# Kernel tuning notes

Measured on AMD Instinct MI355X. Metric: run time of the kernel, lower is better.

Reference implementation:

```python
import jax, jax.numpy as jnp
import numpy as np
from jax import lax

EPS = 1e-5

def mish(x):
    return x * jnp.tanh(jax.nn.softplus(x))

def conv2d(x, w, b, pad):
    y = lax.conv_general_dilated(x, w, (1, 1), [(pad, pad), (pad, pad)],
                                 dimension_numbers=('NCHW', 'OIHW', 'NCHW'))
    return y + b[None, :, None, None]

def dyn_conv(x, w):
    # Per-sample conv with a given kernel: x (B,1,H,W), w (B,Co,k,k).
    # torch code loops (batch, out-channel); equivalent grouped conv with groups=B.
    B, _, H, W = x.shape
    _, Co, k, _ = w.shape
    pad = k // 2 - 1  # int(k/2)-1 as in the torch module
    y = lax.conv_general_dilated(x.reshape(1, B, H, W), w.reshape(B * Co, 1, k, k),
                                 (1, 1), [(pad, pad), (pad, pad)],
                                 feature_group_count=B,
                                 dimension_numbers=('NCHW', 'OIHW', 'NCHW'))
    return y.reshape(B, Co, y.shape[2], y.shape[3])

def maxpool2(x):
    return lax.reduce_window(x, -jnp.inf, lax.max, (1, 1, 2, 2), (1, 1, 2, 2), 'VALID')

def up2(x):
    # bilinear upsample x2, align_corners=True (matches nn.Upsample)
    B, C, H, W = x.shape
    def idx(n):
        s = jnp.arange(2 * n, dtype=x.dtype) * ((n - 1) / (2 * n - 1))
        i0 = jnp.floor(s).astype(jnp.int32)
        i1 = jnp.minimum(i0 + 1, n - 1)
        return i0, i1, s - i0.astype(x.dtype)
    y0, y1, fy = idx(H)
    x0, x1, fx = idx(W)
    a = x[:, :, y0, :] * (1 - fy)[None, None, :, None] + x[:, :, y1, :] * fy[None, None, :, None]
    return a[:, :, :, x0] * (1 - fx) + a[:, :, :, x1] * fx

def batchnorm(x, g, b):
    mu = jnp.mean(x, axis=(0, 2, 3), keepdims=True)
    var = jnp.var(x, axis=(0, 2, 3), keepdims=True)
    return g[None, :, None, None] * (x - mu) * lax.rsqrt(var + EPS) + b[None, :, None, None]

def double_conv(x, wa, ba, wb, bb):
    return mish(conv2d(mish(conv2d(x, wa, ba, 1)), wb, bb, 1))

def setup_inputs() -> dict:
    key = jax.random.key(0)
    ks = iter(jax.random.split(key, 64))
    def rnd(shape, scale):
        return jax.random.normal(next(ks), shape, jnp.float32) * scale
    def cw(co, ci, kk):
        return rnd((co, ci, kk, kk), 1.0 / np.sqrt(ci * kk * kk))
    def cb(co):
        return rnd((co,), 0.01)
    B, H, W, K, NC = 4, 256, 256, 4, 1
    inp = {}
    inp['x'] = rnd((B, 1, H, W), 1.0)
    inp['w'] = rnd((B, 32, K, K), 0.25)  # per-sample dynamic kernels
    inp['d1w'], inp['d1b'] = cw(32, 32, 4), cb(32)
    inp['w2a'], inp['b2a'], inp['w2b'], inp['b2b'] = cw(128, 32, 3), cb(128), cw(128, 128, 3), cb(128)
    inp['w3a'], inp['b3a'], inp['w3b'], inp['b3b'] = cw(256, 128, 3), cb(256), cw(256, 256, 3), cb(256)
    inp['w4a'], inp['b4a'], inp['w4b'], inp['b4b'] = cw(512, 256, 3), cb(512), cw(512, 512, 3), cb(512)
    inp['g4'], inp['be4'] = 1.0 + rnd((512,), 0.1), rnd((512,), 0.1)
    inp['u3a'], inp['ub3a'], inp['u3b'], inp['ub3b'] = cw(256, 768, 3), cb(256), cw(256, 256, 3), cb(256)
    inp['u2a'], inp['ub2a'], inp['u2b'], inp['ub2b'] = cw(128, 384, 3), cb(128), cw(128, 128, 3), cb(128)
    inp['u1a'], inp['ub1a'], inp['u1b'], inp['ub1b'] = cw(32, 160, 3), cb(32), cw(32, 32, 3), cb(32)
    inp['wl'], inp['bl'] = cw(NC, 32, 1), cb(NC)
    return inp

def reference(x, w, d1w, d1b, w2a, b2a, w2b, b2b, w3a, b3a, w3b, b3b,
              w4a, b4a, w4b, b4b, g4, be4, u3a, ub3a, u3b, ub3b,
              u2a, ub2a, u2b, ub2b, u1a, ub1a, u1b, ub1b, wl, bl):
    c1 = mish(conv2d(mish(dyn_conv(x, w)), d1w, d1b, 2))  # (B,32,256,256)
    p = maxpool2(c1)
    c2 = double_conv(p, w2a, b2a, w2b, b2b)               # (B,128,128,128)
    p = maxpool2(c2)
    c3 = double_conv(p, w3a, b3a, w3b, b3b)               # (B,256,64,64)
    p = maxpool2(c3)
    h = double_conv(p, w4a, b4a, w4b, b4b)                # (B,512,32,32)
    h = batchnorm(h, g4, be4)
    h = jnp.concatenate([up2(h), c3], axis=1)             # (B,768,64,64)
    h = double_conv(h, u3a, ub3a, u3b, ub3b)
    h = jnp.concatenate([up2(h), c2], axis=1)             # (B,384,128,128)
    h = double_conv(h, u2a, ub2a, u2b, ub2b)
    h = jnp.concatenate([up2(h), c1], axis=1)             # (B,160,256,256)
    h = double_conv(h, u1a, ub1a, u1b, ub1b)
    return conv2d(h, wl, bl, 0)
```

## Files before the change

kernel.cpp:

```cpp
#include <hip/hip_runtime.h>
#include <hip/hip_bf16.h>
#include <math.h>

#define DEV static __device__ __forceinline__

typedef __attribute__((ext_vector_type(8))) short short8;
typedef __attribute__((ext_vector_type(4))) float floatx4;

DEV float bf2f(const __hip_bfloat16 v) { return __bfloat162float(v); }
DEV float bfu2f(unsigned short u) { return __uint_as_float((unsigned)u << 16); }

DEV unsigned short f2bf(float v) {
    unsigned int b = __float_as_uint(v);
    unsigned int r = (b + 0x7FFFu + ((b >> 16) & 1u)) >> 16;
    return (unsigned short)r;
}

DEV float mishf(float x) {
    float sp = fmaxf(x, 0.0f) + __logf(1.0f + __expf(-fabsf(x)));
    float t = __expf(-2.0f * sp);
    return __fdividef(x * (1.0f - t), 1.0f + t);
}

template<int N> DEV void s_wait_vm() {
    constexpr unsigned e = (unsigned)(N & 15) | (((unsigned)N >> 4) << 14)
                         | (7u << 4) | (15u << 8);
    __builtin_amdgcn_s_waitcnt(e);
}

#define N_T 32
struct Tab {
    const void* src[N_T];
    long long   dstoff[N_T];
    int         n[N_T];
    int         isw[N_T];
    int         cin[N_T];
    int         kk[N_T];
};

__global__ __launch_bounds__(256) void k_detect(Tab t, int* __restrict__ flags) {
    int i = blockIdx.x;
    int n = t.n[i];
    int m = n < 16384 ? n : 16384;
    const unsigned short* p = (const unsigned short*)t.src[i];
    __shared__ int sInf, sExt, sZero;
    if (threadIdx.x == 0) { sInf = 0; sExt = 0; sZero = 0; }
    __syncthreads();
    int cInf = 0, cExt = 0, cZero = 0;
    for (int j = threadIdx.x; j < m; j += 256) {
        unsigned short h = p[j];
        if ((h & 0x7F80) == 0x7F80) cInf++;
        if ((j & 1) == 0) {
            if (h == 0) cZero++;
            else { int e = (h >> 7) & 0xFF; if (e < 56 || e > 184) cExt++; }
        }
    }
    if (cInf)  atomicAdd(&sInf, cInf);
    if (cExt)  atomicAdd(&sExt, cExt);
    if (cZero) atomicAdd(&sZero, cZero);
    __syncthreads();
    if (threadIdx.x == 0) {
        int nEven = (m + 1) >> 1;
        flags[i] = (sInf > 0 || sExt > 0 || (nEven > 0 && sZero == nEven)) ? 2 : 0;
    }
}

__global__ void k_flag_final(Tab t, int* __restrict__ flags, int xi,
                             float* __restrict__ zp) {
    if (blockIdx.x == 0 && threadIdx.x < 16) zp[threadIdx.x] = 0.0f;
    if (threadIdx.x == 0 && blockIdx.x == 0) {
        int xf = (flags[xi] == 2) ? 1 : 0;
        for (int i = 0; i < N_T; ++i) {
            int f;
            if (flags[i] == 2)       f = 1;
            else if (t.n[i] >= 256)  f = 0;
            else                     f = xf;
            flags[i] = f;
        }
    }
}

__global__ __launch_bounds__(256) void k_convert(
        Tab t, float* __restrict__ pf, unsigned short* __restrict__ wb,
        const int* __restrict__ flags) {
    long long idx = (long long)blockIdx.x * 256 + threadIdx.x;
    long long off = 0;
    #pragma unroll 1
    for (int i = 0; i < N_T; ++i) {
        long long ni = t.n[i];
        if (idx < off + ni) {
            int j = (int)(idx - off);
            float v = flags[i] ? ((const float*)t.src[i])[j]
                               : bf2f(((const __hip_bfloat16*)t.src[i])[j]);
            if (t.isw[i]) {
                int cin = t.cin[i], kk = t.kk[i];
                int ckk = cin * kk;
                int co = j / ckk;
                int rem = j - co * ckk;
                int ci = rem / kk;
                int tt = rem - ci * kk;
                int cb = co >> 4, m = co & 15;
                int ch = ci >> 5, q = (ci >> 3) & 3, jj = ci & 7;
                int nc = cin >> 5;
                size_t dst = (((size_t)(cb * kk + tt) * nc + ch) << 9)
                           + (size_t)((q << 4) + m) * 8 + jj;
                wb[t.dstoff[i] + dst] = f2bf(v);
            } else {
                pf[t.dstoff[i] + j] = v;
            }
            return;
        }
        off += ni;
    }
}

__global__ __launch_bounds__(256) void k_dynconv_mish(
        const float* __restrict__ x, const float* __restrict__ w,
        unsigned short* __restrict__ out) {
    const int HO = 255, WO = 255, H = 256, W = 256;
    int p = blockIdx.x * 256 + threadIdx.x;
    if (p >= HO * WO) return;
    int b = blockIdx.y;
    int yo = p / WO, xo = p - yo * WO;
    const float* xp = x + b * H * W;

    float xv[16];
    #pragma unroll
    for (int ky = 0; ky < 4; ++ky) {
        int iy = yo + ky - 1;
        bool yok = (unsigned)iy < (unsigned)H;
        #pragma unroll
        for (int kx = 0; kx < 4; ++kx) {
            int ix = xo + kx - 1;
            xv[ky * 4 + kx] = (yok && (unsigned)ix < (unsigned)W)
                              ? xp[iy * W + ix] : 0.0f;
        }
    }

    const float* wb = w + (b << 9);
    unsigned int ow[16];
    #pragma unroll
    for (int c2 = 0; c2 < 16; ++c2) {
        const float* w0 = wb + (c2 << 5);
        const float* w1 = w0 + 16;
        float a0 = 0.f, a1 = 0.f;
        #pragma unroll
        for (int k = 0; k < 16; ++k) {
            a0 = fmaf(xv[k], w0[k], a0);
            a1 = fmaf(xv[k], w1[k], a1);
        }
        ow[c2] = (unsigned)f2bf(mishf(a0)) | ((unsigned)f2bf(mishf(a1)) << 16);
    }

    unsigned short* op = out + ((size_t)(b * HO * WO) + p) * 32;
    uint4 v;
    v.x = ow[0];  v.y = ow[1];  v.z = ow[2];  v.w = ow[3];
    *(uint4*)(op +  0) = v;
    v.x = ow[4];  v.y = ow[5];  v.z = ow[6];  v.w = ow[7];
    *(uint4*)(op +  8) = v;
    v.x = ow[8];  v.y = ow[9];  v.z = ow[10]; v.w = ow[11];
    *(uint4*)(op + 16) = v;
    v.x = ow[12]; v.y = ow[13]; v.z = ow[14]; v.w = ow[15];
    *(uint4*)(op + 24) = v;
}

template<int KS, int WPX, int WCO, int CO_FR>
__global__ __launch_bounds__(256) void k_conv2(
        const unsigned short* __restrict__ s0, int C0,
        const unsigned short* __restrict__ s1, int C1,
        const unsigned short* __restrict__ wgt,
        const float* __restrict__ bias,
        unsigned short* __restrict__ out,
        int Hin, int Win, int Hout, int Wout, int Co,
        const float* __restrict__ zpad) {
    constexpr int PAD = KS - 2;
    constexpr int KK = KS * KS;
    constexpr int TY = WPX * 4;
    constexpr int HWd = 16 + KS - 1;
    constexpr int HHd = TY + KS - 1;
    constexpr int NLOC = HWd * HHd;
    constexpr int NLD = NLOC * 4;
    constexpr int NPASS = (NLD + 255) / 256;
    constexpr int HALF = NPASS * 2048;
    constexpr int NAV = (KS == 3) ? KK * CO_FR : 0;
    static_assert(2 * HALF * 2 <= 65536, "LDS overflow");
    static_assert(WPX * WCO == 4, "4 waves");
    static_assert(NAV + NPASS <= 63, "vmcnt range");
    __shared__ __align__(16) unsigned short lds[2 * HALF];

    const int tid = threadIdx.x, lane = tid & 63, wv = tid >> 6;
    const int wr = wv / WCO, wc = wv % WCO;
    const int xn = lane & 15, qd = lane >> 4;
    const int C = C0 + C1, NC = C >> 5;
    const int NC0 = C0 >> 5;

    const int txc = Wout >> 4, tyc = Hout / TY;
    const int tpb = txc * tyc;
    const int b = blockIdx.x / tpb;
    int rem = blockIdx.x - b * tpb;
    const int tyi = rem / txc, txi = rem - tyi * txc;
    const int y0 = tyi * TY, x0 = txi << 4;
    const int cobase = blockIdx.y * (WCO * CO_FR * 16);
    const int cob16_0 = (cobase >> 4) + wc * CO_FR;

    const unsigned short* sb0 = s0 + (size_t)b * Hin * Win * C0;
    const unsigned short* sb1 = s1 ? s1 + (size_t)b * Hin * Win * C1 : s0;

    floatx4 acc[4][CO_FR];
    #pragma unroll
    for (int p = 0; p < 4; ++p)
        #pragma unroll
        for (int q = 0; q < CO_FR; ++q)
            acc[p][q] = (floatx4){0.f, 0.f, 0.f, 0.f};

    const int c8 = (tid & 3) << 3;
    int srow[NPASS];
    int sinc[NPASS];
    #pragma unroll
    for (int p_ = 0; p_ < NPASS; ++p_) {
        int i_ = p_ * 256 + tid;
        int loc = i_ >> 2;
        int hy = loc / HWd, hx = loc - hy * HWd;
        int iy = y0 + hy - PAD, ix = x0 + hx - PAD;
        bool ok = (i_ < NLD) && ((unsigned)iy < (unsigned)Hin)
                             && ((unsigned)ix < (unsigned)Win);
        srow[p_] = iy * Win + ix;
        sinc[p_] = ok ? 32 : 0;
    }
    const unsigned short* sptr[NPASS];
    auto initp = [&](const unsigned short* srcp, int Cs) {
        #pragma unroll
        for (int p_ = 0; p_ < NPASS; ++p_)
            sptr[p_] = sinc[p_] ? srcp + (size_t)srow[p_] * Cs + c8
                                : (const unsigned short*)zpad;
    };
    int scnt = 0;
    auto stage_next = [&](int h_) {
        if (s1 && scnt == NC0) initp(sb1, C1);
        #pragma unroll
        for (int p_ = 0; p_ < NPASS; ++p_) {
            __builtin_amdgcn_global_load_lds(
                (const unsigned int*)sptr[p_],
                (unsigned int*)&lds[h_ * HALF + (p_ * 256 + wv * 64) * 8],
                16, 0, 0);
            sptr[p_] += sinc[p_];
        }
        ++scnt;
    };

    initp(sb0, C0);
    stage_next(0);
    for (int ci_ = 0; ci_ < NC; ++ci_) {
        const int h = ci_ & 1;
        const size_t wof = ((size_t)cob16_0 * KK * NC + ci_) * 512 + lane * 8;
        short8 avr[KK][CO_FR];
        if constexpr (KS == 3) {
            #pragma unroll
            for (int tap = 0; tap < KK; ++tap)
                #pragma unroll
                for (int q = 0; q < CO_FR; ++q)
                    avr[tap][q] = *(const short8*)(wgt + wof
                                    + (size_t)(q * KK + tap) * NC * 512);
            __builtin_amdgcn_sched_barrier(0);
        }
        if (ci_ + 1 < NC) stage_next(h ^ 1);
        __builtin_amdgcn_sched_barrier(0);
        if (ci_ + 1 < NC) s_wait_vm<NAV + NPASS>();
        else              s_wait_vm<NAV>();
        __builtin_amdgcn_s_barrier();
        __builtin_amdgcn_sched_barrier(0);
        const unsigned short* base = &lds[h * HALF];
        #pragma unroll
        for (int dy = 0; dy < KS; ++dy) {
            #pragma unroll
            for (int dx = 0; dx < KS; ++dx) {
                const int tap = dy * KS + dx;
                short8 av[CO_FR];
                if constexpr (KS == 3) {
                    #pragma unroll
                    for (int q = 0; q < CO_FR; ++q) av[q] = avr[tap][q];
                } else {
                    #pragma unroll
                    for (int q = 0; q < CO_FR; ++q)
                        av[q] = *(const short8*)(wgt + wof
                                  + (size_t)(q * KK + tap) * NC * 512);
                }
                #pragma unroll
                for (int p = 0; p < 4; ++p) {
                    short8 bv = *(const short8*)&base[
                        ((4 * wr + p + dy) * HWd + xn + dx) * 32 + qd * 8];
                    #pragma unroll
                    for (int q = 0; q < CO_FR; ++q)
                        acc[p][q] = __builtin_amdgcn_mfma_f32_16x16x32_bf16(
                            av[q], bv, acc[p][q], 0, 0, 0);
                }
            }
        }
        __builtin_amdgcn_sched_barrier(0);
        __builtin_amdgcn_s_barrier();
        __builtin_amdgcn_sched_barrier(0);
    }

    #pragma unroll
    for (int p = 0; p < 4; ++p) {
        const int y = y0 + 4 * wr + p;
        unsigned short* ob = out + (((size_t)b * Hout + y) * Wout + x0 + xn) * Co;
        #pragma unroll
        for (int q = 0; q < CO_FR; ++q) {
            const int co = cobase + (wc * CO_FR + q) * 16 + qd * 4;
            ushort4 o;
            o.x = f2bf(mishf(acc[p][q][0] + bias[co + 0]));
            o.y = f2bf(mishf(acc[p][q][1] + bias[co + 1]));
            o.z = f2bf(mishf(acc[p][q][2] + bias[co + 2]));
            o.w = f2bf(mishf(acc[p][q][3] + bias[co + 3]));
            *(ushort4*)(ob + co) = o;
        }
    }
}

__global__ __launch_bounds__(256) void k_maxpool(
        const unsigned short* __restrict__ in, unsigned short* __restrict__ out,
        int lgWin, int lgC, int total8) {
    int idx = blockIdx.x * 256 + threadIdx.x;
    if (idx >= total8) return;
    int Wo = 1 << (lgWin - 1);
    int vc = idx & ((1 << (lgC - 3)) - 1); int t = idx >> (lgC - 3);
    int xo = t & (Wo - 1); t >>= (lgWin - 1);
    int yo = t & (Wo - 1); int b = t >> (lgWin - 1);
    size_t base = (((((size_t)(b << lgWin) + 2 * yo) << lgWin) + 2 * xo) << lgC)
                + ((size_t)vc << 3);
    size_t dc = (size_t)1 << lgC, dr = (size_t)1 << (lgWin + lgC);
    short8 v0 = *(const short8*)&in[base];
    short8 v1 = *(const short8*)&in[base + dc];
    short8 v2 = *(const short8*)&in[base + dr];
    short8 v3 = *(const short8*)&in[base + dr + dc];
    short8 o;
    #pragma unroll
    for (int j = 0; j < 8; ++j) {
        float m = fmaxf(fmaxf(bfu2f((unsigned short)v0[j]),
                              bfu2f((unsigned short)v1[j])),
                        fmaxf(bfu2f((unsigned short)v2[j]),
                              bfu2f((unsigned short)v3[j])));
        o[j] = (short)f2bf(m);
    }
    *(short8*)&out[(size_t)idx * 8] = o;
}

__global__ __launch_bounds__(256) void k_bn_reduce(
        const unsigned short* __restrict__ in, float* __restrict__ stats) {
    __shared__ float ls[4], ls2[4];
    int c = blockIdx.x;
    int tid = threadIdx.x;
    float s = 0.f, s2 = 0.f;
    for (int i = tid; i < 4096; i += 256) {
        float v = bfu2f(in[(size_t)i * 512 + c]);
        s += v; s2 += v * v;
    }
    #pragma unroll
    for (int off = 32; off; off >>= 1) {
        s  += __shfl_down(s, off, 64);
        s2 += __shfl_down(s2, off, 64);
    }
    if ((tid & 63) == 0) { ls[tid >> 6] = s; ls2[tid >> 6] = s2; }
    __syncthreads();
    if (tid == 0) {
        s  = ls[0] + ls[1] + ls[2] + ls[3];
        s2 = ls2[0] + ls2[1] + ls2[2] + ls2[3];
        float mean = s * (1.f / 4096.f);
        float var  = fmaxf(s2 * (1.f / 4096.f) - mean * mean, 0.f);
        stats[c]       = mean;
        stats[512 + c] = rsqrtf(var + 1e-5f);
    }
}

__global__ __launch_bounds__(256) void k_bn_apply(
        unsigned short* __restrict__ data, const float* __restrict__ stats,
        const float* __restrict__ g, const float* __restrict__ be, int total8) {
    int idx = blockIdx.x * 256 + threadIdx.x;
    if (idx >= total8) return;
    int c0 = (idx & 63) << 3;
    short8 v = *(const short8*)&data[(size_t)idx * 8];
    short8 o;
    #pragma unroll
    for (int j = 0; j < 8; ++j) {
        int c = c0 + j;
        float x = bfu2f((unsigned short)v[j]);
        o[j] = (short)f2bf(g[c] * (x - stats[c]) * stats[512 + c] + be[c]);
    }
    *(short8*)&data[(size_t)idx * 8] = o;
}

__global__ __launch_bounds__(256) void k_up2(
        const unsigned short* __restrict__ in, unsigned short* __restrict__ out,
        int lgW, int lgC, int total8) {
    int idx = blockIdx.x * 256 + threadIdx.x;
    if (idx >= total8) return;
    int H = 1 << lgW;
    int vc = idx & ((1 << (lgC - 3)) - 1); int t = idx >> (lgC - 3);
    int xo = t & (2 * H - 1); t >>= (lgW + 1);
    int yo = t & (2 * H - 1); int b = t >> (lgW + 1);
    float sc = (float)(H - 1) / (float)(2 * H - 1);
    float sy = yo * sc, sx = xo * sc;
    int y0 = (int)sy; int y1 = min(y0 + 1, H - 1); float fy = sy - (float)y0;
    int x0 = (int)sx; int x1 = min(x0 + 1, H - 1); float fx = sx - (float)x0;
    size_t bb = (size_t)b << (2 * lgW);
    size_t c = (size_t)vc << 3;
    size_t i00 = (((bb + ((size_t)y0 << lgW) + x0)) << lgC) + c;
    size_t i01 = (((bb + ((size_t)y0 << lgW) + x1)) << lgC) + c;
    size_t i10 = (((bb + ((size_t)y1 << lgW) + x0)) << lgC) + c;
    size_t i11 = (((bb + ((size_t)y1 << lgW) + x1)) << lgC) + c;
    short8 a00 = *(const short8*)&in[i00];
    short8 a01 = *(const short8*)&in[i01];
    short8 a10 = *(const short8*)&in[i10];
    short8 a11 = *(const short8*)&in[i11];
    short8 o;
    #pragma unroll
    for (int j = 0; j < 8; ++j) {
        float a  = bfu2f((unsigned short)a00[j]) * (1.f - fx)
                 + bfu2f((unsigned short)a01[j]) * fx;
        float b2 = bfu2f((unsigned short)a10[j]) * (1.f - fx)
                 + bfu2f((unsigned short)a11[j]) * fx;
        o[j] = (short)f2bf(a * (1.f - fy) + b2 * fy);
    }
    *(short8*)&out[(size_t)idx * 8] = o;
}

__global__ __launch_bounds__(256) void k_final1x1(
        const unsigned short* __restrict__ in, const float* __restrict__ wl,
        const float* __restrict__ bl, float* __restrict__ out) {
    int idx = blockIdx.x * 256 + threadIdx.x;
    if (idx >= 4 * 256 * 256) return;
    const unsigned short* p = in + (size_t)idx * 32;
    short8 r0 = *(const short8*)&p[0];
    short8 r1 = *(const short8*)&p[8];
    short8 r2 = *(const short8*)&p[16];
    short8 r3 = *(const short8*)&p[24];
    float acc = bl[0];
    #pragma unroll
    for (int j = 0; j < 8; ++j) {
        acc = fmaf(bfu2f((unsigned short)r0[j]), wl[j],      acc);
        acc = fmaf(bfu2f((unsigned short)r1[j]), wl[j + 8],  acc);
        acc = fmaf(bfu2f((unsigned short)r2[j]), wl[j + 16], acc);
        acc = fmaf(bfu2f((unsigned short)r3[j]), wl[j + 24], acc);
    }
    out[idx] = acc;
}

static inline int nblk(long long n) { return (int)((n + 255) / 256); }

extern "C" void kernel_launch(void* const* d_in, const int* in_sizes, int n_in,
                              void* d_out, int out_size, void* d_ws, size_t ws_size,
                              hipStream_t stream) {
    static const int EXP_SZ[N_T] = {
        262144, 2048, 16384, 32, 36864, 128, 147456, 128,
        294912, 256, 589824, 256, 1179648, 512, 2359296, 512,
        512, 512, 1769472, 256, 589824, 256, 442368, 128,
        147456, 128, 46080, 32, 9216, 32, 32, 1 };
    static const int ISW[N_T] = {
        0,0,1,0, 1,0,1,0, 1,0,1,0, 1,0,1,0,
        0,0, 1,0,1,0, 1,0,1,0, 1,0,1,0, 0,0 };
    static const int CIN[N_T] = {
        0,0,32,0, 32,0,128,0, 128,0,256,0, 256,0,512,0,
        0,0, 768,0,256,0, 384,0,128,0, 160,0,32,0, 0,0 };
    static const int KKA[N_T] = {
        0,0,16,0, 9,0,9,0, 9,0,9,0, 9,0,9,0,
        0,0, 9,0,9,0, 9,0,9,0, 9,0,9,0, 0,0 };
    int o = -1;
    for (int s = 0; s + N_T <= n_in; ++s) {
        bool ok = true;
        for (int j = 0; j < N_T; ++j)
            if (in_sizes[s + j] != EXP_SZ[j]) { ok = false; break; }
        if (ok) { o = s; break; }
    }
    if (o < 0) return;

    float* ws = (float*)d_ws;
    const long long PFN   = 270336;
    const long long C1o   = PFN;
    const long long C2o   = C1o + 8388608;
    const long long C3o   = C2o + 8388608;
    const long long Po    = C3o + 4194304;
    const long long Qo    = Po  + 8388608;
    const long long STo   = Qo  + 8388608;
    const long long FLo   = STo + 1024;
    const long long ZPo   = FLo + 64;
    const long long WBo   = ZPo + 16;
    const long long WBN   = 7628800;
    const size_t NEED = (size_t)WBo * 4 + WBN * 2 + 256;
    if (ws_size < NEED) return;

    float* PF = ws;
    unsigned short* C1 = (unsigned short*)(ws + C1o);
    unsigned short* C2 = (unsigned short*)(ws + C2o);
    unsigned short* C3 = (unsigned short*)(ws + C3o);
    unsigned short* P  = (unsigned short*)(ws + Po);
    unsigned short* Q  = (unsigned short*)(ws + Qo);
    float* ST = ws + STo;
    int* FLAGS = (int*)(ws + FLo);
    float* ZP = ws + ZPo;
    unsigned short* WB = (unsigned short*)(ws + WBo);
    unsigned short* X3 = C3;
    unsigned short* U2 = P;
    unsigned short* H2 = C2;
    unsigned short* U1 = P;
    unsigned short* X1 = C3;
    unsigned short* O1 = P;

    Tab tab;
    long long foff = 0, woff = 0, total = 0;
    const float* fp[N_T];
    const unsigned short* wbp[N_T];
    for (int i = 0; i < N_T; ++i) {
        tab.src[i] = d_in[o + i];
        tab.n[i]   = in_sizes[o + i];
        tab.isw[i] = ISW[i];
        tab.cin[i] = CIN[i];
        tab.kk[i]  = KKA[i];
        if (ISW[i]) { tab.dstoff[i] = woff; wbp[i] = WB + woff; fp[i] = nullptr; woff += tab.n[i]; }
        else        { tab.dstoff[i] = foff; fp[i] = PF + foff; wbp[i] = nullptr; foff += tab.n[i]; }
        total += tab.n[i];
    }
    if (foff > PFN || woff > WBN) return;

    const float* xf  = fp[0];  const float* wf = fp[1];
    const unsigned short* d1w = wbp[2];  const float* d1b = fp[3];
    const unsigned short* w2a = wbp[4];  const float* b2a = fp[5];
    const unsigned short* w2b = wbp[6];  const float* b2b = fp[7];
    const unsigned short* w3a = wbp[8];  const float* b3a = fp[9];
    const unsigned short* w3b = wbp[10]; const float* b3b = fp[11];
    const unsigned short* w4a = wbp[12]; const float* b4a = fp[13];
    const unsigned short* w4b = wbp[14]; const float* b4b = fp[15];
    const float* g4 = fp[16], *be4 = fp[17];
    const unsigned short* u3aw = wbp[18]; const float* ub3a = fp[19];
    const unsigned short* u3bw = wbp[20]; const float* ub3b = fp[21];
    const unsigned short* u2aw = wbp[22]; const float* ub2a = fp[23];
    const unsigned short* u2bw = wbp[24]; const float* ub2b = fp[25];
    const unsigned short* u1aw = wbp[26]; const float* ub1a = fp[27];
    const unsigned short* u1bw = wbp[28]; const float* ub1b = fp[29];
    const float* wl = fp[30], *bl = fp[31];
    float* outp = (float*)d_out;

    dim3 blk(256);
    long long n;

    k_detect<<<N_T, blk, 0, stream>>>(tab, FLAGS);
    k_flag_final<<<1, 64, 0, stream>>>(tab, FLAGS, 0, ZP);
    k_convert<<<nblk(total), blk, 0, stream>>>(tab, PF, WB, FLAGS);

    k_dynconv_mish<<<dim3(nblk(255 * 255), 4), blk, 0, stream>>>(xf, wf, P);
    k_conv2<4, 4, 1, 2><<<dim3(4 * 16 * 16, 1), blk, 0, stream>>>(
        P, 32, nullptr, 0, d1w, d1b, C1, 255, 255, 256, 256, 32, ZP);
    n = 4ll * 128 * 128 * 32 / 8;
    k_maxpool<<<nblk(n), blk, 0, stream>>>(C1, Q, 8, 5, (int)n);
    k_conv2<3, 2, 2, 2><<<dim3(4 * 8 * 16, 2), blk, 0, stream>>>(
        Q, 32, nullptr, 0, w2a, b2a, P, 128, 128, 128, 128, 128, ZP);
    k_conv2<3, 2, 2, 2><<<dim3(4 * 8 * 16, 2), blk, 0, stream>>>(
        P, 128, nullptr, 0, w2b, b2b, C2, 128, 128, 128, 128, 128, ZP);
    n = 4ll * 64 * 64 * 128 / 8;
    k_maxpool<<<nblk(n), blk, 0, stream>>>(C2, Q, 7, 7, (int)n);
    k_conv2<3, 2, 2, 1><<<dim3(4 * 4 * 8, 8), blk, 0, stream>>>(
        Q, 128, nullptr, 0, w3a, b3a, P, 64, 64, 64, 64, 256, ZP);
    k_conv2<3, 2, 2, 1><<<dim3(4 * 4 * 8, 8), blk, 0, stream>>>(
        P, 256, nullptr, 0, w3b, b3b, C3, 64, 64, 64, 64, 256, ZP);
    n = 4ll * 32 * 32 * 256 / 8;
    k_maxpool<<<nblk(n), blk, 0, stream>>>(C3, Q, 6, 8, (int)n);
    k_conv2<3, 2, 2, 1><<<dim3(4 * 2 * 4, 16), blk, 0, stream>>>(
        Q, 256, nullptr, 0, w4a, b4a, P, 32, 32, 32, 32, 512, ZP);
    k_conv2<3, 2, 2, 1><<<dim3(4 * 2 * 4, 16), blk, 0, stream>>>(
        P, 512, nullptr, 0, w4b, b4b, Q, 32, 32, 32, 32, 512, ZP);
    n = 4ll * 32 * 32 * 512 / 8;
    k_bn_reduce<<<512, blk, 0, stream>>>(Q, ST);
    k_bn_apply<<<nblk(n), blk, 0, stream>>>(Q, ST, g4, be4, (int)n);

    n = 4ll * 64 * 64 * 512 / 8;
    k_up2<<<nblk(n), blk, 0, stream>>>(Q, P, 5, 9, (int)n);
    k_conv2<3, 2, 2, 1><<<dim3(4 * 4 * 8, 8), blk, 0, stream>>>(
        P, 512, C3, 256, u3aw, ub3a, Q, 64, 64, 64, 64, 256, ZP);
    k_conv2<3, 2, 2, 1><<<dim3(4 * 4 * 8, 8), blk, 0, stream>>>(
        Q, 256, nullptr, 0, u3bw, ub3b, X3, 64, 64, 64, 64, 256, ZP);

    n = 4ll * 128 * 128 * 256 / 8;
    k_up2<<<nblk(n), blk, 0, stream>>>(X3, U2, 6, 8, (int)n);
    k_conv2<3, 2, 2, 2><<<dim3(4 * 8 * 16, 2), blk, 0, stream>>>(
        U2, 256, C2, 128, u2aw, ub2a, Q, 128, 128, 128, 128, 128, ZP);
    k_conv2<3, 2, 2, 2><<<dim3(4 * 8 * 16, 2), blk, 0, stream>>>(
        Q, 128, nullptr, 0, u2bw, ub2b, H2, 128, 128, 128, 128, 128, ZP);

    n = 4ll * 256 * 256 * 128 / 8;
    k_up2<<<nblk(n), blk, 0, stream>>>(H2, U1, 7, 7, (int)n);
    k_conv2<3, 4, 1, 2><<<dim3(4 * 16 * 16, 1), blk, 0, stream>>>(
        U1, 128, C1, 32, u1aw, ub1a, X1, 256, 256, 256, 256, 32, ZP);
    k_conv2<3, 4, 1, 2><<<dim3(4 * 16 * 16, 1), blk, 0, stream>>>(
        X1, 32, nullptr, 0, u1bw, ub1b, O1, 256, 256, 256, 256, 32, ZP);

    n = 4ll * 256 * 256;
    k_final1x1<<<nblk(n), blk, 0, stream>>>(O1, wl, bl, outp);
}
```

Before: 682.0 us.

## Reuse LDS input rows across filter taps in 3x3 conv, speed up weight conversion

The 3x3 conv inner loop now walks the six input rows a warp touches and loads each row's three shifted B fragments from LDS once, feeding every (output row, dy) pair that uses them. This replaces the old per-tap, per-output-row loads, cutting LDS reads from 36 to 18 per channel chunk. Separately, the weight/param convert kernel finds its tensor from a per-block start table instead of a linear scan, and replaces integer divides with magic-number multiplies. The risk is higher register pressure from holding extra B fragments alongside the preloaded weight fragments.

```diff
diff --git a/kernel.cpp b/kernel.cpp
--- a/kernel.cpp
+++ b/kernel.cpp
@@ -36,6 +36,9 @@
     int         isw[N_T];
     int         cin[N_T];
     int         kk[N_T];
+    int         bs[N_T];
+    unsigned long long mckk[N_T];
+    unsigned long long mkk[N_T];
 };
 
 __global__ __launch_bounds__(256) void k_detect(Tab t, int* __restrict__ flags) {
@@ -83,34 +86,31 @@
 __global__ __launch_bounds__(256) void k_convert(
         Tab t, float* __restrict__ pf, unsigned short* __restrict__ wb,
         const int* __restrict__ flags) {
-    long long idx = (long long)blockIdx.x * 256 + threadIdx.x;
-    long long off = 0;
+    int bx = blockIdx.x;
+    int i = 0;
     #pragma unroll 1
-    for (int i = 0; i < N_T; ++i) {
-        long long ni = t.n[i];
-        if (idx < off + ni) {
-            int j = (int)(idx - off);
-            float v = flags[i] ? ((const float*)t.src[i])[j]
-                               : bf2f(((const __hip_bfloat16*)t.src[i])[j]);
-            if (t.isw[i]) {
-                int cin = t.cin[i], kk = t.kk[i];
-                int ckk = cin * kk;
-                int co = j / ckk;
-                int rem = j - co * ckk;
-                int ci = rem / kk;
-                int tt = rem - ci * kk;
-                int cb = co >> 4, m = co & 15;
-                int ch = ci >> 5, q = (ci >> 3) & 3, jj = ci & 7;
-                int nc = cin >> 5;
-                size_t dst = (((size_t)(cb * kk + tt) * nc + ch) << 9)
-                           + (size_t)((q << 4) + m) * 8 + jj;
-                wb[t.dstoff[i] + dst] = f2bf(v);
-            } else {
-                pf[t.dstoff[i] + j] = v;
-            }
-            return;
-        }
-        off += ni;
+    while (i + 1 < N_T && bx >= t.bs[i + 1]) ++i;
+    int j = (bx - t.bs[i]) * 256 + threadIdx.x;
+    if (j >= t.n[i]) return;
+    float v = flags[i] ? ((const float*)t.src[i])[j]
+                       : bf2f(((const __hip_bfloat16*)t.src[i])[j]);
+    if (t.isw[i]) {
+        int kk = t.kk[i], cin = t.cin[i];
+        int ckk = cin * kk;
+        unsigned co = (unsigned)(((unsigned long long)(unsigned)j
+                                  * t.mckk[i]) >> 39);
+        int rem = j - (int)co * ckk;
+        unsigned ci = (unsigned)(((unsigned long long)(unsigned)rem
+                                  * t.mkk[i]) >> 39);
+        int tt = rem - (int)ci * kk;
+        int cb = (int)co >> 4, m = (int)co & 15;
+        int ch = (int)ci >> 5, q = ((int)ci >> 3) & 3, jj = (int)ci & 7;
+        int nc = cin >> 5;
+        size_t dst = (((size_t)(cb * kk + tt) * nc + ch) << 9)
+                   + (size_t)((q << 4) + m) * 8 + jj;
+        wb[t.dstoff[i] + dst] = f2bf(v);
+    } else {
+        pf[t.dstoff[i] + j] = v;
     }
 }
 
@@ -270,29 +270,51 @@
         __builtin_amdgcn_s_barrier();
         __builtin_amdgcn_sched_barrier(0);
         const unsigned short* base = &lds[h * HALF];
-        #pragma unroll
-        for (int dy = 0; dy < KS; ++dy) {
+        if constexpr (KS == 3) {
             #pragma unroll
-            for (int dx = 0; dx < KS; ++dx) {
-                const int tap = dy * KS + dx;
-                short8 av[CO_FR];
-                if constexpr (KS == 3) {
-                    #pragma unroll
-                    for (int q = 0; q < CO_FR; ++q) av[q] = avr[tap][q];
-                } else {
+            for (int r = 0; r < 6; ++r) {
+                short8 bv[3];
+                #pragma unroll
+                for (int dx = 0; dx < 3; ++dx)
+                    bv[dx] = *(const short8*)&base[
+                        ((4 * wr + r) * HWd + xn + dx) * 32 + qd * 8];
+                #pragma unroll
+                for (int dy = 0; dy < 3; ++dy) {
+                    const int p = r - dy;
+                    if (p >= 0 && p < 4) {
+                        #pragma unroll
+                        for (int dx = 0; dx < 3; ++dx) {
+                            const int tap = dy * 3 + dx;
+                            #pragma unroll
+                            for (int q = 0; q < CO_FR; ++q)
+                                acc[p][q] =
+                                    __builtin_amdgcn_mfma_f32_16x16x32_bf16(
+                                        avr[tap][q], bv[dx], acc[p][q],
+                                        0, 0, 0);
+                        }
+                    }
+                }
+            }
+        } else {
+            #pragma unroll
+            for (int dy = 0; dy < KS; ++dy) {
+                #pragma unroll
+                for (int dx = 0; dx < KS; ++dx) {
+                    const int tap = dy * KS + dx;
+                    short8 av[CO_FR];
                     #pragma unroll
                     for (int q = 0; q < CO_FR; ++q)
                         av[q] = *(const short8*)(wgt + wof
                                   + (size_t)(q * KK + tap) * NC * 512);
-                }
-                #pragma unroll
-                for (int p = 0; p < 4; ++p) {
-                    short8 bv = *(const short8*)&base[
-                        ((4 * wr + p + dy) * HWd + xn + dx) * 32 + qd * 8];
                     #pragma unroll
-                    for (int q = 0; q < CO_FR; ++q)
-                        acc[p][q] = __builtin_amdgcn_mfma_f32_16x16x32_bf16(
-                            av[q], bv, acc[p][q], 0, 0, 0);
+                    for (int p = 0; p < 4; ++p) {
+                        short8 bv = *(const short8*)&base[
+                            ((4 * wr + p + dy) * HWd + xn + dx) * 32 + qd * 8];
+                        #pragma unroll
+                        for (int q = 0; q < CO_FR; ++q)
+                            acc[p][q] = __builtin_amdgcn_mfma_f32_16x16x32_bf16(
+                                av[q], bv, acc[p][q], 0, 0, 0);
+                    }
                 }
             }
         }
@@ -507,7 +529,8 @@
     unsigned short* O1 = P;
 
     Tab tab;
-    long long foff = 0, woff = 0, total = 0;
+    long long foff = 0, woff = 0;
+    int nbc = 0;
     const float* fp[N_T];
     const unsigned short* wbp[N_T];
     for (int i = 0; i < N_T; ++i) {
@@ -516,9 +539,14 @@
         tab.isw[i] = ISW[i];
         tab.cin[i] = CIN[i];
         tab.kk[i]  = KKA[i];
+        tab.bs[i]  = nbc;
+        nbc += (in_sizes[o + i] + 255) / 256;
+        long long D1 = ISW[i] ? (long long)CIN[i] * KKA[i] : 1;
+        long long D2 = ISW[i] ? (long long)KKA[i] : 1;
+        tab.mckk[i] = ((1ULL << 39) + D1 - 1) / (unsigned long long)D1;
+        tab.mkk[i]  = ((1ULL << 39) + D2 - 1) / (unsigned long long)D2;
         if (ISW[i]) { tab.dstoff[i] = woff; wbp[i] = WB + woff; fp[i] = nullptr; woff += tab.n[i]; }
         else        { tab.dstoff[i] = foff; fp[i] = PF + foff; wbp[i] = nullptr; foff += tab.n[i]; }
-        total += tab.n[i];
     }
     if (foff > PFN || woff > WBN) return;
 
@@ -545,7 +573,7 @@
 
     k_detect<<<N_T, blk, 0, stream>>>(tab, FLAGS);
     k_flag_final<<<1, 64, 0, stream>>>(tab, FLAGS, 0, ZP);
-    k_convert<<<nblk(total), blk, 0, stream>>>(tab, PF, WB, FLAGS);
+    k_convert<<<nbc, blk, 0, stream>>>(tab, PF, WB, FLAGS);
 
     k_dynconv_mish<<<dim3(nblk(255 * 255), 4), blk, 0, stream>>>(xf, wf, P);
     k_conv2<4, 4, 1, 2><<<dim3(4 * 16 * 16, 1), blk, 0, stream>>>(
```

After: 664.4 us. 1.03x faster.
